# Performance work log

Measured on AMD Instinct MI355X. Metric: run time of the kernel, lower is better.

## Reference

```python
import jax, jax.numpy as jnp
import numpy as np

IN_F, H1, H2, NC = 784, 1024, 1024, 10
BATCH = 32
EPS = 0.1


def setup_inputs() -> dict:
    key = jax.random.key(0)
    ks = jax.random.split(key, 8)
    x = jax.random.normal(ks[0], (BATCH, IN_F), jnp.float32)
    y = jax.random.randint(ks[1], (BATCH,), 0, NC)
    W1 = jax.random.normal(ks[2], (H1, IN_F), jnp.float32) / np.float32(np.sqrt(IN_F))
    b1 = jax.random.normal(ks[3], (H1,), jnp.float32) * 0.01
    W2 = jax.random.normal(ks[4], (H2, H1), jnp.float32) / np.float32(np.sqrt(H1))
    b2 = jax.random.normal(ks[5], (H2,), jnp.float32) * 0.01
    W3 = jax.random.normal(ks[6], (NC, H2), jnp.float32) / np.float32(np.sqrt(H2))
    b3 = jax.random.normal(ks[7], (NC,), jnp.float32) * 0.01
    return dict(x=x, y=y, W1=W1, b1=b1, W2=W2, b2=b2, W3=W3, b3=b3)


def _relu_coeffs(zl, zu):
    # d = 1 where zl>=0, zu/(zu-zl) where crossing, 0 where zu<=0 (as in select_layer)
    I = (zl < 0) & (zu > 0)
    d = jnp.where(zl >= 0, 1.0, jnp.where(I, zu / (zu - zl), 0.0))
    lI = jnp.where(I, zl, 0.0)  # zl restricted to crossing set I
    return d, lI


def reference(x, y, W1, b1, W2, b2, W3, b3):
    eps = jnp.float32(EPS)
    # ---- layer-1 preactivation bounds (InfBall fval) ----
    nom1 = x @ W1.T + b1                              # [B,H1]
    r1 = eps * jnp.abs(W1).sum(1)                     # [H1]
    zl1, zu1 = nom1 - r1, nom1 + r1
    d1, l1m = _relu_coeffs(zl1, zu1)                  # [B,H1]

    # ---- layer-2 preactivation bounds via dual (transpose) propagation, nu = I ----
    nu1 = W2[None, :, :] * d1[:, None, :]             # [B,H2,H1]  (D1 W2^T rows)
    V0 = jnp.einsum('bji,ik->bjk', nu1, W1)           # [B,H2,IN]
    A = jnp.einsum('bjk,bk->bj', V0, x) + b2 + nu1 @ b1
    E = eps * jnp.abs(V0).sum(-1)
    crossl = jnp.einsum('bji,bi->bj', jax.nn.relu(-nu1), l1m)
    crossu = jnp.einsum('bji,bi->bj', jax.nn.relu(nu1), l1m)
    zl2 = A - E + crossl
    zu2 = A + E - crossu
    d2, l2m = _relu_coeffs(zl2, zu2)                  # [B,H2]

    # ---- final robust bounds: c[b,j,:] = e_{y_b} - e_j ----
    eye = jnp.eye(NC, dtype=x.dtype)
    c = eye[y][:, None, :] - eye[None, :, :]          # [B,NC,NC]
    nu2 = (c @ W3) * d2[:, None, :]                   # [B,NC,H2]
    nu1f = (nu2 @ W2) * d1[:, None, :]                # [B,NC,H1]
    V0f = nu1f @ W1                                   # [B,NC,IN]
    Af = jnp.einsum('bjk,bk->bj', V0f, x) + c @ b3 + nu2 @ b2 + nu1f @ b1
    Ef = eps * jnp.abs(V0f).sum(-1)
    crossf = (jnp.einsum('bji,bi->bj', jax.nn.relu(-nu2), l2m)
              + jnp.einsum('bji,bi->bj', jax.nn.relu(-nu1f), l1m))
    J = Af - Ef + crossf                              # lower bound of c^T z
    return -J                                         # f: upper bound of z_j - z_y, [B,NC]
```

## Files before the change

kernel.cpp:

```cpp
#include <hip/hip_runtime.h>
#include <math.h>

#define B    32
#define INF  784
#define H1   1024
#define H2   1024
#define NC   10
#define EPSV 0.1f

typedef __attribute__((ext_vector_type(8))) short short8;
typedef __attribute__((ext_vector_type(4))) float floatx4;

__device__ inline ushort bf16_rne(float f) {
  uint u = __builtin_bit_cast(uint, f);
  u += 0x7FFFu + ((u >> 16) & 1u);
  return (ushort)(u >> 16);
}
__device__ inline uint pack2(float a, float b) {
  return (uint)bf16_rne(a) | ((uint)bf16_rne(b) << 16);
}
__device__ inline uint scale_pack(uint u, float d0, float d1v) {
  float f0 = __builtin_bit_cast(float, u << 16) * d0;
  float f1 = __builtin_bit_cast(float, u & 0xFFFF0000u) * d1v;
  uint r0 = __builtin_bit_cast(uint, f0) + 0x8000u;
  uint r1 = __builtin_bit_cast(uint, f1) + 0x8000u;
  return __builtin_amdgcn_perm(r1, r0, 0x07060302u);
}

__global__ __launch_bounds__(256) void k_pre(
    const float* __restrict__ x, const float* __restrict__ W1,
    const float* __restrict__ b1, const float* __restrict__ W2,
    ushort* __restrict__ W1F, ushort* __restrict__ W2F,
    float* __restrict__ d1B, float* __restrict__ t1B, float* __restrict__ dnB,
    float* __restrict__ Ezero)
{
  __shared__ float red[4][B + 1];
  __shared__ float Ts[4][32][17];
  int bid = blockIdx.x;
  int t = threadIdx.x;
  if (bid < 64) {
    int jt = bid;
    int lane = t & 63, c0 = t >> 6;
    int l15 = lane & 15, quad = lane >> 4;
    for (int c = c0; c < 32; c += 4) {
      const float* src = &W2[(size_t)(jt * 16 + l15) * H1 + c * 32 + quad * 8];
      float4 v0 = *reinterpret_cast<const float4*>(src);
      float4 v1 = *reinterpret_cast<const float4*>(src + 4);
      uint4 o;
      o.x = pack2(v0.x, v0.y); o.y = pack2(v0.z, v0.w);
      o.z = pack2(v1.x, v1.y); o.w = pack2(v1.z, v1.w);
      *reinterpret_cast<uint4*>(&W2F[((size_t)(c * 64 + jt) * 64 + lane) * 8]) = o;
    }
  } else if (bid < 116) {
    int mt = bid - 64;
    int w = t >> 6, lane = t & 63;
    int l15 = lane & 15, quad = lane >> 4;
    if (mt >= 49) {
      uint4 z; z.x = 0; z.y = 0; z.z = 0; z.w = 0;
      for (int cg = 0; cg < 8; cg++) {
        int c = cg * 4 + w;
        *reinterpret_cast<uint4*>(&W1F[((size_t)(c * 52 + mt) * 64 + lane) * 8]) = z;
      }
    } else {
      int col0 = mt * 16;
      for (int cg = 0; cg < 8; cg++) {
        int c = cg * 4 + w;
#pragma unroll
        for (int p = 0; p < 8; p++) {
          int r = p * 4 + (lane >> 4);
          Ts[w][r][lane & 15] = W1[(size_t)(c * 32 + r) * INF + col0 + (lane & 15)];
        }
        float f[8];
#pragma unroll
        for (int e = 0; e < 8; e++) f[e] = Ts[w][quad * 8 + e][l15];
        uint4 o;
        o.x = pack2(f[0], f[1]); o.y = pack2(f[2], f[3]);
        o.z = pack2(f[4], f[5]); o.w = pack2(f[6], f[7]);
        *reinterpret_cast<uint4*>(&W1F[((size_t)(c * 52 + mt) * 64 + lane) * 8]) = o;
      }
    }
  } else if (bid < 1140) {
    int i = bid - 116;
    const float* w = W1 + (size_t)i * INF;
    float acc[B];
#pragma unroll
    for (int b = 0; b < B; b++) acc[b] = 0.f;
    float wabs = 0.f;
    for (int k = t; k < INF; k += 256) {
      float wv = w[k];
      wabs += fabsf(wv);
#pragma unroll
      for (int b = 0; b < B; b++) acc[b] = fmaf(x[b * INF + k], wv, acc[b]);
    }
#pragma unroll
    for (int off = 32; off > 0; off >>= 1) {
#pragma unroll
      for (int b = 0; b < B; b++) acc[b] += __shfl_down(acc[b], off, 64);
      wabs += __shfl_down(wabs, off, 64);
    }
    int wave = t >> 6, lane = t & 63;
    if (lane == 0) {
#pragma unroll
      for (int b = 0; b < B; b++) red[wave][b] = acc[b];
      red[wave][B] = wabs;
    }
    __syncthreads();
    if (t < B) {
      float s = red[0][t] + red[1][t] + red[2][t] + red[3][t];
      float r = EPSV * (red[0][B] + red[1][B] + red[2][B] + red[3][B]);
      float nom = s + b1[i];
      float zl = nom - r, zu = nom + r;
      float d, l;
      if (zl >= 0.f)      { d = 1.f;            l = 0.f; }
      else if (zu > 0.f)  { d = zu / (zu - zl); l = zl;  }
      else                { d = 0.f;            l = 0.f; }
      d1B[(size_t)t * H1 + i] = d;
      t1B[(size_t)t * H1 + i] = d * l;
      dnB[(size_t)t * H1 + i] = d * nom;
    }
  } else {
    int zb = bid - 1140;
    for (int idx = t; idx < 8192; idx += 256) {
      int pos = zb * 8192 + idx;
      if (pos < 54272) Ezero[pos] = 0.f;
    }
  }
}

#define K3_LOAD(c, A, Bv) do {                                                  \
  Bv = *reinterpret_cast<const uint4*>(bBase + (size_t)(c) * 32768);            \
  _Pragma("unroll")                                                             \
  for (int mi = 0; mi < 13; mi++)                                               \
    A[mi] = *reinterpret_cast<const uint4*>(aBase + (size_t)(c) * 26624 + mi * 512); \
} while (0)

#define K3F_COMP(c, A, Bv, DsRow, accB) do {                                    \
  float4 dv0 = *reinterpret_cast<const float4*>(&DsRow[(c) * 32]);              \
  float4 dv1 = *reinterpret_cast<const float4*>(&DsRow[(c) * 32 + 4]);          \
  uint4 sb;                                                                     \
  sb.x = scale_pack(Bv.x, dv0.x, dv0.y);                                        \
  sb.y = scale_pack(Bv.y, dv0.z, dv0.w);                                        \
  sb.z = scale_pack(Bv.z, dv1.x, dv1.y);                                        \
  sb.w = scale_pack(Bv.w, dv1.z, dv1.w);                                        \
  short8 bfr = __builtin_bit_cast(short8, sb);                                  \
  _Pragma("unroll")                                                             \
  for (int mi = 0; mi < 13; mi++)                                               \
    accB[mi] = __builtin_amdgcn_mfma_f32_16x16x32_bf16(                         \
        __builtin_bit_cast(short8, A[mi]), bfr, accB[mi], 0, 0, 0);             \
} while (0)

__global__ __launch_bounds__(256, 2) void k3(
    const ushort* __restrict__ W1F, const ushort* __restrict__ W2F,
    const float* __restrict__ d1B, float* __restrict__ E)
{
  int b0 = blockIdx.z * 2;
  int t = threadIdx.x, w = t >> 6, lane = t & 63;
  int quad = lane >> 4, l15 = lane & 15;
  int mt0 = blockIdx.x * 13;
  int jt = blockIdx.y * 4 + w;

  __shared__ float Ds[2][H1];
  for (int idx = t; idx < 2 * H1; idx += 256)
    Ds[idx >> 10][idx & 1023] = d1B[(size_t)(b0 + (idx >> 10)) * H1 + (idx & 1023)];
  __syncthreads();

  const ushort* aBase = W1F + ((size_t)mt0 * 64 + lane) * 8;
  const ushort* bBase = W2F + ((size_t)jt * 64 + lane) * 8;
  const float* Ds0 = &Ds[0][quad * 8];
  const float* Ds1 = &Ds[1][quad * 8];

  floatx4 acc[2][13];
#pragma unroll
  for (int bb = 0; bb < 2; bb++)
#pragma unroll
    for (int mi = 0; mi < 13; mi++) acc[bb][mi] = (floatx4){0.f, 0.f, 0.f, 0.f};

  uint4 a0[13], a1[13], b0v, b1v;
  K3_LOAD(0, a0, b0v);
  K3_LOAD(1, a1, b1v);
  for (int c = 0; c < 30; c += 2) {
    K3F_COMP(c, a0, b0v, Ds0, acc[0]);
    K3F_COMP(c, a0, b0v, Ds1, acc[1]);
    K3_LOAD(c + 2, a0, b0v);
    K3F_COMP(c + 1, a1, b1v, Ds0, acc[0]);
    K3F_COMP(c + 1, a1, b1v, Ds1, acc[1]);
    if (c + 3 < 32) K3_LOAD(c + 3, a1, b1v);
  }
  K3F_COMP(30, a0, b0v, Ds0, acc[0]);
  K3F_COMP(30, a0, b0v, Ds1, acc[1]);
  K3F_COMP(31, a1, b1v, Ds0, acc[0]);
  K3F_COMP(31, a1, b1v, Ds1, acc[1]);

#pragma unroll
  for (int bb = 0; bb < 2; bb++) {
    float s = 0.f;
#pragma unroll
    for (int mi = 0; mi < 13; mi++)
#pragma unroll
      for (int r = 0; r < 4; r++) s += fabsf(acc[bb][mi][r]);
    s += __shfl_xor(s, 16, 64);
    s += __shfl_xor(s, 32, 64);
    if (lane < 16) {
      int j = jt * 16 + l15;
      atomicAdd(&E[(size_t)j * B + b0 + bb], EPSV * s);
    }
  }
}

__global__ __launch_bounds__(256) void k245a(
    const float* __restrict__ W2, const float* __restrict__ b2,
    const float* __restrict__ dnB, const float* __restrict__ t1B,
    const float* __restrict__ E, const float* __restrict__ W3,
    const int* __restrict__ y,
    float* __restrict__ nu2T, float* __restrict__ F2)
{
  int j = blockIdx.x;
  int t = threadIdx.x;
  int wave = t >> 6, lane = t & 63;
  int b0 = wave * 8;
  float aA[8] = {}, aCl[8] = {}, aCu[8] = {};
  const float* __restrict__ w2 = W2 + (size_t)j * H1;
  for (int i = lane; i < H1; i += 64) {
    float wv = w2[i];
    float wp = fmaxf(wv, 0.f), wn = fmaxf(-wv, 0.f);
#pragma unroll
    for (int r = 0; r < 8; r++) {
      float dv = dnB[(size_t)(b0 + r) * H1 + i];
      float tv = t1B[(size_t)(b0 + r) * H1 + i];
      aA[r]  = fmaf(wv, dv, aA[r]);
      aCl[r] = fmaf(wn, tv, aCl[r]);
      aCu[r] = fmaf(wp, tv, aCu[r]);
    }
  }
#pragma unroll
  for (int off = 32; off > 0; off >>= 1) {
#pragma unroll
    for (int r = 0; r < 8; r++) {
      aA[r]  += __shfl_down(aA[r],  off, 64);
      aCl[r] += __shfl_down(aCl[r], off, 64);
      aCu[r] += __shfl_down(aCu[r], off, 64);
    }
  }
  __shared__ float sA[B], sCl[B], sCu[B];
  __shared__ float sd2[B], st2[B], sdb[B], swy[B], sw3[NC];
  float bj = b2[j];
  if (lane == 0) {
#pragma unroll
    for (int r = 0; r < 8; r++) {
      sA [b0 + r] = aA[r] + bj;
      sCl[b0 + r] = aCl[r];
      sCu[b0 + r] = aCu[r];
    }
  }
  if (t >= 64 && t < 96)   swy[t - 64]  = W3[(size_t)y[t - 64] * H2 + j];
  if (t >= 128 && t < 138) sw3[t - 128] = W3[(size_t)(t - 128) * H2 + j];
  __syncthreads();
  if (t < B) {
    float a = sA[t], e = E[(size_t)j * B + t];
    float zl = a - e + sCl[t];
    float zu = a + e - sCu[t];
    float d, l;
    if (zl >= 0.f)      { d = 1.f;            l = 0.f; }
    else if (zu > 0.f)  { d = zu / (zu - zl); l = zl;  }
    else                { d = 0.f;            l = 0.f; }
    sd2[t] = d;
    st2[t] = d * l;
    sdb[t] = d * bj;
  }
  __syncthreads();
  for (int tt = t; tt < B * NC; tt += 256) {
    int b = tt / NC, jc = tt - b * NC;
    float cw = swy[b] - sw3[jc];
    float d2v = sd2[b];
    nu2T[((size_t)b * H2 + j) * 12 + jc] = cw * d2v;
    float val = cw * sdb[b] + fmaxf(-cw, 0.f) * st2[b];
    atomicAdd(&F2[((size_t)(j & 63) * B + b) * NC + jc], val);
  }
}

__global__ __launch_bounds__(256) void k5b1(
    const float* __restrict__ W2, const float* __restrict__ nu2T,
    float* __restrict__ hpart)
{
  int t = threadIdx.x;
  int i1 = blockIdx.x * 512 + t * 2;
  int b = blockIdx.y, s = blockIdx.z;
  const float* __restrict__ nrowb = nu2T + ((size_t)b * H2 + s * 128) * 12;
  const float* __restrict__ w2b = W2 + (size_t)s * 128 * H1 + i1;
  float h0[NC] = {}, h1[NC] = {};
  for (int i2 = 0; i2 < 128; i2++) {
    float2 wv = *reinterpret_cast<const float2*>(&w2b[(size_t)i2 * H1]);
    const float* __restrict__ nrow = nrowb + i2 * 12;
#pragma unroll
    for (int j = 0; j < NC; j++) {
      h0[j] = fmaf(nrow[j], wv.x, h0[j]);
      h1[j] = fmaf(nrow[j], wv.y, h1[j]);
    }
  }
#pragma unroll
  for (int j = 0; j < NC; j++) {
    float2 o; o.x = h0[j]; o.y = h1[j];
    *reinterpret_cast<float2*>(&hpart[(((size_t)s * B + b) * NC + j) * H1 + i1]) = o;
  }
}

__global__ __launch_bounds__(256) void k5b2(
    const float* __restrict__ hpart,
    const float* __restrict__ d1B, const float* __restrict__ t1B,
    const float* __restrict__ dnB,
    float* __restrict__ nu1fT, float* __restrict__ F)
{
  int t = threadIdx.x;
  int i1 = blockIdx.x * 256 + t;
  int b = blockIdx.y;
  float d1v = d1B[(size_t)b * H1 + i1];
  float t1v = t1B[(size_t)b * H1 + i1];
  float dnv = dnB[(size_t)b * H1 + i1];
  float sn[NC], c1[NC];
#pragma unroll
  for (int j = 0; j < NC; j++) {
    float hv = 0.f;
#pragma unroll
    for (int s = 0; s < 8; s++)
      hv += hpart[(((size_t)s * B + b) * NC + j) * H1 + i1];
    nu1fT[((size_t)b * H1 + i1) * 12 + j] = hv * d1v;
    sn[j] = hv * dnv;
    c1[j] = fmaxf(-hv, 0.f) * t1v;
  }
#pragma unroll
  for (int off = 32; off > 0; off >>= 1) {
#pragma unroll
    for (int j = 0; j < NC; j++) {
      sn[j] += __shfl_down(sn[j], off, 64);
      c1[j] += __shfl_down(c1[j], off, 64);
    }
  }
  __shared__ float red[4][2 * NC];
  int wave = t >> 6, lane = t & 63;
  if (lane == 0) {
#pragma unroll
    for (int j = 0; j < NC; j++) { red[wave][j] = sn[j]; red[wave][NC + j] = c1[j]; }
  }
  __syncthreads();
  if (t < NC) {
    float s = 0.f;
    for (int w = 0; w < 4; w++) s += red[w][t] + red[w][NC + t];
    atomicAdd(&F[b * NC + t], s);
  }
}

__global__ __launch_bounds__(128) void k5c1(
    const float* __restrict__ W1, const float* __restrict__ nu1fT,
    float* __restrict__ ppart)
{
  int t = threadIdx.x;
  bool valid = (t < 112);
  int k = blockIdx.x * 112 + (valid ? t : 0);
  int b = blockIdx.y, s = blockIdx.z;
  const float* __restrict__ nrowb = nu1fT + ((size_t)b * H1 + s * 128) * 12;
  const float* __restrict__ w1b = W1 + (size_t)s * 128 * INF + k;
  float acc[NC] = {};
  for (int i1 = 0; i1 < 128; i1++) {
    float w1v = w1b[(size_t)i1 * INF];
    const float* __restrict__ nrow = nrowb + i1 * 12;
#pragma unroll
    for (int j = 0; j < NC; j++) acc[j] = fmaf(nrow[j], w1v, acc[j]);
  }
  if (valid) {
#pragma unroll
    for (int j = 0; j < NC; j++)
      ppart[(((size_t)s * B + b) * NC + j) * INF + k] = acc[j];
  }
}

__global__ __launch_bounds__(256) void k5c2_out(
    const float* __restrict__ ppart, const float* __restrict__ F,
    const float* __restrict__ F2, const float* __restrict__ b3,
    const int* __restrict__ y, float* __restrict__ out)
{
  int b = blockIdx.x;
  int t = threadIdx.x;
  float e[NC] = {};
  for (int k = t; k < INF; k += 256) {
#pragma unroll
    for (int j = 0; j < NC; j++) {
      float v = 0.f;
#pragma unroll
      for (int s = 0; s < 8; s++)
        v += ppart[(((size_t)s * B + b) * NC + j) * INF + k];
      e[j] += fabsf(v);
    }
  }
#pragma unroll
  for (int off = 32; off > 0; off >>= 1) {
#pragma unroll
    for (int j = 0; j < NC; j++) e[j] += __shfl_down(e[j], off, 64);
  }
  __shared__ float red[4][NC];
  int wave = t >> 6, lane = t & 63;
  if (lane == 0) {
#pragma unroll
    for (int j = 0; j < NC; j++) red[wave][j] = e[j];
  }
  __syncthreads();
  if (t < NC) {
    float ef = 0.f;
    for (int w = 0; w < 4; w++) ef += red[w][t];
    float s = F[b * NC + t];
    for (int slot = 0; slot < 64; slot++)
      s += F2[((size_t)slot * B + b) * NC + t];
    int yb = y[b];
    s += b3[yb] - b3[t];
    out[b * NC + t] = EPSV * ef - s;
  }
}

extern "C" void kernel_launch(void* const* d_in, const int* in_sizes, int n_in,
                              void* d_out, int out_size, void* d_ws, size_t ws_size,
                              hipStream_t stream) {
  const float* x  = (const float*)d_in[0];
  const int*   y  = (const int*)  d_in[1];
  const float* W1 = (const float*)d_in[2];
  const float* b1 = (const float*)d_in[3];
  const float* W2 = (const float*)d_in[4];
  const float* b2 = (const float*)d_in[5];
  const float* W3 = (const float*)d_in[6];
  const float* b3 = (const float*)d_in[7];
  float* out = (float*)d_out;
  float* ws  = (float*)d_ws;

  float* d1B  = ws;
  float* t1B  = ws + 32768;
  float* dnB  = ws + 65536;
  float* E    = ws + 196608;
  float* F    = ws + 229376;
  float* F2   = ws + 230400;
  float* nu2T = ws + 328704;
  ushort* W2F = (ushort*)(ws + 721920);
  ushort* W1F = (ushort*)(ws + 1246208);
  float* nu1fT = ws + 328704;
  float* hpart = ws + 721920;
  float* ppart = ws + 721920;

  k_pre<<<1147, 256, 0, stream>>>(x, W1, b1, W2, W1F, W2F, d1B, t1B, dnB, E);
  k3<<<dim3(4, 16, 16), 256, 0, stream>>>(W1F, W2F, d1B, E);
  k245a<<<H2, 256, 0, stream>>>(W2, b2, dnB, t1B, E, W3, y, nu2T, F2);
  k5b1<<<dim3(2, B, 8), 256, 0, stream>>>(W2, nu2T, hpart);
  k5b2<<<dim3(4, B), 256, 0, stream>>>(hpart, d1B, t1B, dnB, nu1fT, F);
  k5c1<<<dim3(7, B, 8), 128, 0, stream>>>(W1, nu1fT, ppart);
  k5c2_out<<<B, 256, 0, stream>>>(ppart, F, F2, b3, y, out);
}
```

Baseline: 219.1 us.

## Stage shared W1 tiles in LDS via global_load_lds double buffering in k3

Previously each of the four waves in a k3 block separately loaded the same 13 W1 fragments into registers. Now the waves split that load and issue it with global_load_lds DMA into a double-buffered LDS tile, then read fragments from LDS for the MFMAs. Launch bounds rise to 3 blocks per CU since the A-fragment registers are freed. In exchange the loop gains two block barriers per iteration and about 26KB of LDS per block. There is also a possible ordering concern: the DMA may not be complete when the barrier is reached.

```diff
diff --git a/kernel.cpp b/kernel.cpp
--- a/kernel.cpp
+++ b/kernel.cpp
@@ -25,6 +25,12 @@
   uint r0 = __builtin_bit_cast(uint, f0) + 0x8000u;
   uint r1 = __builtin_bit_cast(uint, f1) + 0x8000u;
   return __builtin_amdgcn_perm(r1, r0, 0x07060302u);
+}
+
+typedef __attribute__((address_space(1))) const unsigned int g_as1;
+typedef __attribute__((address_space(3))) unsigned int l_as3;
+__device__ __forceinline__ void gll16(const void* g, void* l) {
+  __builtin_amdgcn_global_load_lds((g_as1*)g, (l_as3*)l, 16, 0, 0);
 }
 
 __global__ __launch_bounds__(256) void k_pre(
@@ -127,44 +133,48 @@
   }
 }
 
-#define K3_LOAD(c, A, Bv) do {                                                  \
-  Bv = *reinterpret_cast<const uint4*>(bBase + (size_t)(c) * 32768);            \
+#define K3_ISSUE(c, buf) do {                                                   \
+  for (int mi = w; mi < 13; mi += 4)                                            \
+    gll16(W1F + (((size_t)(c) * 52 + mtBase + mi) * 64 + lane) * 8,             \
+          &Abuf[buf][mi * 64]);                                                 \
+} while (0)
+
+#define K3_SCALE(bv, DsRow, cc, bfr) do {                                       \
+  float4 dv0 = *reinterpret_cast<const float4*>(&DsRow[(cc) * 32]);             \
+  float4 dv1 = *reinterpret_cast<const float4*>(&DsRow[(cc) * 32 + 4]);         \
+  uint4 sb;                                                                     \
+  sb.x = scale_pack(bv.x, dv0.x, dv0.y);                                        \
+  sb.y = scale_pack(bv.y, dv0.z, dv0.w);                                        \
+  sb.z = scale_pack(bv.z, dv1.x, dv1.y);                                        \
+  sb.w = scale_pack(bv.w, dv1.z, dv1.w);                                        \
+  bfr = __builtin_bit_cast(short8, sb);                                         \
+} while (0)
+
+#define K3_MFMA(buf, bf0, bf1) do {                                             \
   _Pragma("unroll")                                                             \
-  for (int mi = 0; mi < 13; mi++)                                               \
-    A[mi] = *reinterpret_cast<const uint4*>(aBase + (size_t)(c) * 26624 + mi * 512); \
+  for (int mi = 0; mi < 13; mi++) {                                             \
+    short8 af = *reinterpret_cast<const short8*>(&Abuf[buf][mi * 64 + lane]);   \
+    acc[0][mi] = __builtin_amdgcn_mfma_f32_16x16x32_bf16(af, bf0, acc[0][mi], 0, 0, 0); \
+    acc[1][mi] = __builtin_amdgcn_mfma_f32_16x16x32_bf16(af, bf1, acc[1][mi], 0, 0, 0); \
+  }                                                                             \
 } while (0)
 
-#define K3F_COMP(c, A, Bv, DsRow, accB) do {                                    \
-  float4 dv0 = *reinterpret_cast<const float4*>(&DsRow[(c) * 32]);              \
-  float4 dv1 = *reinterpret_cast<const float4*>(&DsRow[(c) * 32 + 4]);          \
-  uint4 sb;                                                                     \
-  sb.x = scale_pack(Bv.x, dv0.x, dv0.y);                                        \
-  sb.y = scale_pack(Bv.y, dv0.z, dv0.w);                                        \
-  sb.z = scale_pack(Bv.z, dv1.x, dv1.y);                                        \
-  sb.w = scale_pack(Bv.w, dv1.z, dv1.w);                                        \
-  short8 bfr = __builtin_bit_cast(short8, sb);                                  \
-  _Pragma("unroll")                                                             \
-  for (int mi = 0; mi < 13; mi++)                                               \
-    accB[mi] = __builtin_amdgcn_mfma_f32_16x16x32_bf16(                         \
-        __builtin_bit_cast(short8, A[mi]), bfr, accB[mi], 0, 0, 0);             \
-} while (0)
-
-__global__ __launch_bounds__(256, 2) void k3(
+__global__ __launch_bounds__(256, 3) void k3(
     const ushort* __restrict__ W1F, const ushort* __restrict__ W2F,
     const float* __restrict__ d1B, float* __restrict__ E)
 {
   int b0 = blockIdx.z * 2;
   int t = threadIdx.x, w = t >> 6, lane = t & 63;
   int quad = lane >> 4, l15 = lane & 15;
-  int mt0 = blockIdx.x * 13;
   int jt = blockIdx.y * 4 + w;
+  int mtBase = blockIdx.x * 13;
 
   __shared__ float Ds[2][H1];
+  __shared__ uint4 Abuf[2][13 * 64];
+
   for (int idx = t; idx < 2 * H1; idx += 256)
     Ds[idx >> 10][idx & 1023] = d1B[(size_t)(b0 + (idx >> 10)) * H1 + (idx & 1023)];
-  __syncthreads();
-
-  const ushort* aBase = W1F + ((size_t)mt0 * 64 + lane) * 8;
+
   const ushort* bBase = W2F + ((size_t)jt * 64 + lane) * 8;
   const float* Ds0 = &Ds[0][quad * 8];
   const float* Ds1 = &Ds[1][quad * 8];
@@ -175,21 +185,31 @@
 #pragma unroll
     for (int mi = 0; mi < 13; mi++) acc[bb][mi] = (floatx4){0.f, 0.f, 0.f, 0.f};
 
-  uint4 a0[13], a1[13], b0v, b1v;
-  K3_LOAD(0, a0, b0v);
-  K3_LOAD(1, a1, b1v);
-  for (int c = 0; c < 30; c += 2) {
-    K3F_COMP(c, a0, b0v, Ds0, acc[0]);
-    K3F_COMP(c, a0, b0v, Ds1, acc[1]);
-    K3_LOAD(c + 2, a0, b0v);
-    K3F_COMP(c + 1, a1, b1v, Ds0, acc[0]);
-    K3F_COMP(c + 1, a1, b1v, Ds1, acc[1]);
-    if (c + 3 < 32) K3_LOAD(c + 3, a1, b1v);
-  }
-  K3F_COMP(30, a0, b0v, Ds0, acc[0]);
-  K3F_COMP(30, a0, b0v, Ds1, acc[1]);
-  K3F_COMP(31, a1, b1v, Ds0, acc[0]);
-  K3F_COMP(31, a1, b1v, Ds1, acc[1]);
+  K3_ISSUE(0, 0);
+  uint4 bv0 = *reinterpret_cast<const uint4*>(bBase);
+  uint4 bv1 = *reinterpret_cast<const uint4*>(bBase + 32768);
+  __syncthreads();
+
+  for (int c = 0; c < 32; c += 2) {
+    if (c + 1 < 32) K3_ISSUE(c + 1, 1);
+    {
+      short8 bf0, bf1;
+      K3_SCALE(bv0, Ds0, c, bf0);
+      K3_SCALE(bv0, Ds1, c, bf1);
+      if (c + 2 < 32) bv0 = *reinterpret_cast<const uint4*>(bBase + (size_t)(c + 2) * 32768);
+      K3_MFMA(0, bf0, bf1);
+    }
+    __syncthreads();
+    if (c + 2 < 32) K3_ISSUE(c + 2, 0);
+    {
+      short8 bf0, bf1;
+      K3_SCALE(bv1, Ds0, c + 1, bf0);
+      K3_SCALE(bv1, Ds1, c + 1, bf1);
+      if (c + 3 < 32) bv1 = *reinterpret_cast<const uint4*>(bBase + (size_t)(c + 3) * 32768);
+      K3_MFMA(1, bf0, bf1);
+    }
+    __syncthreads();
+  }
 
 #pragma unroll
   for (int bb = 0; bb < 2; bb++) {
```

After: 216.6 us. About the same (-1.2%).
